# Kernel optimization log

Hardware: AMD Instinct MI355X
Metric: run time of the kernel (lower is better)

The kernel has to match this reference:

```python
import jax, jax.numpy as jnp
import numpy as np

H = 8          # num_heads
EPS = 1e-5     # nn.LayerNorm default eps


def _attn(x, kv, wq, bq, wk, bk, wv, bv, wo, bo):
    # x: [B, Nq, D] queries; kv: [B, Nk, D] keys/values. softmax over keys (dim=-1).
    B, Nq, D = x.shape
    Nk = kv.shape[1]
    d = D // H
    q = (x @ wq + bq).reshape(B, Nq, H, d).transpose(0, 2, 1, 3)   # [B,h,Nq,d]
    k = (kv @ wk + bk).reshape(B, Nk, H, d).transpose(0, 2, 1, 3)  # [B,h,Nk,d]
    v = (kv @ wv + bv).reshape(B, Nk, H, d).transpose(0, 2, 1, 3)  # [B,h,Nk,d]
    scores = jnp.einsum('bhqd,bhkd->bhqk', q, k) * (d ** -0.5)
    a = jax.nn.softmax(scores, axis=-1)                            # softmax_dim='keys'
    ctx = jnp.einsum('bhqk,bhkd->bhqd', a, v)
    ctx = ctx.transpose(0, 2, 1, 3).reshape(B, Nq, D)
    return ctx @ wo + bo


def _ln(x, g, b):
    mu = jnp.mean(x, axis=-1, keepdims=True)
    var = jnp.var(x, axis=-1, keepdims=True)  # biased, matches torch LayerNorm
    return (x - mu) * jax.lax.rsqrt(var + EPS) * g + b


def setup_inputs() -> dict:
    key = jax.random.key(0)
    B, Nq, Nk, D = 2, 2048, 4096, 512
    Hid = 4 * D
    ks = jax.random.split(key, 32)
    s = 0.02
    r = lambda i, shp: jax.random.normal(ks[i], shp, dtype=jnp.float32) * s
    inp = {
        'x': jax.random.normal(ks[0], (B, Nq, D), dtype=jnp.float32),
        'cross': jax.random.normal(ks[1], (B, Nk, D), dtype=jnp.float32),
        # cross-attention projections (stored as [in, out])
        'ca_wq': r(2, (D, D)), 'ca_bq': jnp.zeros((D,), jnp.float32),
        'ca_wk': r(3, (D, D)), 'ca_bk': jnp.zeros((D,), jnp.float32),
        'ca_wv': r(4, (D, D)), 'ca_bv': jnp.zeros((D,), jnp.float32),
        'ca_wo': r(5, (D, D)), 'ca_bo': jnp.zeros((D,), jnp.float32),
        # self-attention projections
        'sa_wq': r(6, (D, D)), 'sa_bq': jnp.zeros((D,), jnp.float32),
        'sa_wk': r(7, (D, D)), 'sa_bk': jnp.zeros((D,), jnp.float32),
        'sa_wv': r(8, (D, D)), 'sa_bv': jnp.zeros((D,), jnp.float32),
        'sa_wo': r(9, (D, D)), 'sa_bo': jnp.zeros((D,), jnp.float32),
        # layer norms
        'ln1_g': jnp.ones((D,), jnp.float32), 'ln1_b': jnp.zeros((D,), jnp.float32),
        'ln2_g': jnp.ones((D,), jnp.float32), 'ln2_b': jnp.zeros((D,), jnp.float32),
        # MLP
        'mlp_w1': r(10, (D, Hid)), 'mlp_b1': jnp.zeros((Hid,), jnp.float32),
        'mlp_w2': r(11, (Hid, D)), 'mlp_b2': jnp.zeros((D,), jnp.float32),
    }
    return inp


def reference(x, cross,
              ca_wq, ca_bq, ca_wk, ca_bk, ca_wv, ca_bv, ca_wo, ca_bo,
              sa_wq, sa_bq, sa_wk, sa_bk, sa_wv, sa_bv, sa_wo, sa_bo,
              ln1_g, ln1_b, ln2_g, ln2_b,
              mlp_w1, mlp_b1, mlp_w2, mlp_b2):
    # a) cross-attention
    xc = _attn(x, cross, ca_wq, ca_bq, ca_wk, ca_bk, ca_wv, ca_bv, ca_wo, ca_bo)
    # b,c) LN then self-attention (Q=K=V=ln1(xc))
    xn = _ln(xc, ln1_g, ln1_b)
    xs = _attn(xn, xn, sa_wq, sa_bq, sa_wk, sa_bk, sa_wv, sa_bv, sa_wo, sa_bo)
    # d) residual
    y = xc + xs
    # e,f) LN + GELU MLP (torch GELU default = exact erf)
    h1 = jax.nn.gelu(_ln(y, ln2_g, ln2_b) @ mlp_w1 + mlp_b1, approximate=False)
    z = h1 @ mlp_w2 + mlp_b2
    # g) residual
    return y + z
```

## Files before the change

kernel.cpp:

```cpp
#include <hip/hip_runtime.h>
#include <math.h>

typedef _Float16 f16;
typedef __attribute__((ext_vector_type(8))) _Float16 f16x8;
typedef __attribute__((ext_vector_type(4))) _Float16 f16x4;
typedef __attribute__((ext_vector_type(4))) float f32x4;
typedef __attribute__((ext_vector_type(2))) __fp16 h16x2;

#define QSCALE 0.1803368801111204f

__device__ __forceinline__ void gl_lds16(const f16* g, f16* l) {
    __builtin_amdgcn_global_load_lds((const __attribute__((address_space(1))) void*)g,
                                     (__attribute__((address_space(3))) void*)l, 16, 0, 0);
}

struct PrepArgs {
    const float* ws[10]; f16* wd[10];
    const float* x; f16* xh;
    const float* cross; f16* ch;
};
__global__ __launch_bounds__(256)
void prep_all(PrepArgs p) {
    __shared__ float t[32][33];
    int bid = blockIdx.x, tid = threadIdx.x;
    if (bid < 4096) {
        const float* W; f16* Wt; int K, N, nx, ky;
        if (bid < 2048) {
            int wi = bid >> 8, tl = bid & 255;
            W = p.ws[wi]; Wt = p.wd[wi]; K = 512; N = 512; nx = tl & 15; ky = tl >> 4;
        } else if (bid < 3072) {
            int tl = bid - 2048;
            W = p.ws[8]; Wt = p.wd[8]; K = 512; N = 2048; nx = tl & 63; ky = tl >> 6;
        } else {
            int tl = bid - 3072;
            W = p.ws[9]; Wt = p.wd[9]; K = 2048; N = 512; nx = tl & 15; ky = tl >> 4;
        }
        int tx = tid & 31, ty = tid >> 5;
        int n0 = nx * 32, k0 = ky * 32;
#pragma unroll
        for (int i = 0; i < 4; i++)
            t[ty + i * 8][tx] = W[(size_t)(k0 + ty + i * 8) * N + n0 + tx];
        __syncthreads();
#pragma unroll
        for (int i = 0; i < 4; i++)
            Wt[(size_t)(n0 + ty + i * 8) * K + k0 + tx] = (f16)t[tx][ty + i * 8];
    } else {
        const float* X; f16* Y; size_t cb;
        if (bid < 6144) { X = p.x; Y = p.xh; cb = bid - 4096; }
        else            { X = p.cross; Y = p.ch; cb = bid - 6144; }
        size_t i = (cb * 256 + tid) * 4;
        f32x4 v = *(const f32x4*)(X + i);
        f16x4 o;
        o[0] = (f16)v[0]; o[1] = (f16)v[1]; o[2] = (f16)v[2]; o[3] = (f16)v[3];
        *(f16x4*)(Y + i) = o;
    }
}

__global__ __launch_bounds__(256)
void transpose_v(const f16* __restrict__ Vh, f16* __restrict__ Vt, int Nk) {
    __shared__ f16 t[64][72];
    int bh = blockIdx.y, k0 = blockIdx.x * 64;
    int tid = threadIdx.x;
    int kr = tid >> 2, dc = (tid & 3) * 16;
    const f16* src = Vh + ((size_t)bh * Nk + k0 + kr) * 64 + dc;
    f16x8 a = *(const f16x8*)src;
    f16x8 b = *(const f16x8*)(src + 8);
    *(f16x8*)&t[kr][dc] = a;
    *(f16x8*)&t[kr][dc + 8] = b;
    __syncthreads();
    int dr = tid >> 2, kc = (tid & 3) * 16;
    f16x8 o0, o1;
#pragma unroll
    for (int j = 0; j < 8; j++) { o0[j] = t[kc + j][dr]; o1[j] = t[kc + 8 + j][dr]; }
    f16* dst = Vt + ((size_t)bh * 64 + dr) * Nk + k0 + kc;
    *(f16x8*)dst = o0;
    *(f16x8*)(dst + 8) = o1;
}

__global__ __launch_bounds__(128)
void layernorm_f16(const float* __restrict__ X, const float* __restrict__ g,
                   const float* __restrict__ bta, f16* __restrict__ Y)
{
    __shared__ float red[4];
    int row = blockIdx.x;
    int tid = threadIdx.x;
    const float* x = X + (size_t)row * 512;
    f32x4 v = *(const f32x4*)(x + tid * 4);
    float s  = v[0] + v[1] + v[2] + v[3];
    float ss = v[0] * v[0] + v[1] * v[1] + v[2] * v[2] + v[3] * v[3];
#pragma unroll
    for (int m = 1; m < 64; m <<= 1) {
        s  += __shfl_xor(s, m, 64);
        ss += __shfl_xor(ss, m, 64);
    }
    int wave = tid >> 6, lane = tid & 63;
    if (lane == 0) { red[wave * 2] = s; red[wave * 2 + 1] = ss; }
    __syncthreads();
    s = red[0] + red[2]; ss = red[1] + red[3];
    float mu  = s * (1.0f / 512);
    float var = ss * (1.0f / 512) - mu * mu;
    float inv = rsqrtf(var + 1e-5f);
    f32x4 gv = *(const f32x4*)(g + tid * 4);
    f32x4 bv = *(const f32x4*)(bta + tid * 4);
    f16x4 o;
#pragma unroll
    for (int i = 0; i < 4; i++) o[i] = (f16)((v[i] - mu) * inv * gv[i] + bv[i]);
    *(f16x4*)(Y + (size_t)row * 512 + tid * 4) = o;
}

__global__ __launch_bounds__(256)
void gemm_f16(const f16* __restrict__ A, const f16* __restrict__ Wt,
              const float* __restrict__ b0, const float* __restrict__ b1,
              const float* __restrict__ b2, const float* __restrict__ res,
              float* __restrict__ Cf32, f16* __restrict__ C16,
              f16* __restrict__ hm0, f16* __restrict__ hm1, f16* __restrict__ hm2,
              int N, int K, int NBshift, int fused, int act, float s0)
{
    __shared__ __align__(16) f16 As[2][128 * 64];
    __shared__ __align__(16) f16 Bs[2][128 * 64];
    int tid = threadIdx.x, lane = tid & 63, wave = tid >> 6;
    int quad = lane >> 4, ln16 = lane & 15;
    int wm = wave >> 1, wn = wave & 1;
    int bm0 = blockIdx.y * 128, bn0 = blockIdx.x * 128;

    f32x4 acc[4][4];
#pragma unroll
    for (int i = 0; i < 4; i++)
#pragma unroll
        for (int j = 0; j < 4; j++) acc[i][j] = (f32x4){0.f, 0.f, 0.f, 0.f};

    const f16* ag[4]; const f16* bg[4]; int Loff[4];
#pragma unroll
    for (int j = 0; j < 4; j++) {
        int L = tid + j * 256;
        int row = L >> 3, cc = (L & 7) ^ (row & 7);
        ag[j] = A  + (size_t)(bm0 + row) * K + cc * 8;
        bg[j] = Wt + (size_t)(bn0 + row) * K + cc * 8;
        Loff[j] = L * 8;
    }
    int sw0 = (quad ^ (ln16 & 7)) * 8, sw1 = ((4 + quad) ^ (ln16 & 7)) * 8;

#pragma unroll
    for (int j = 0; j < 4; j++) { gl_lds16(ag[j], &As[0][Loff[j]]); gl_lds16(bg[j], &Bs[0][Loff[j]]); }
#pragma unroll
    for (int j = 0; j < 4; j++) { ag[j] += 64; bg[j] += 64; }

    int cur = 0;
    for (int kt = 0; kt < K; kt += 64) {
        __syncthreads();
        if (kt + 64 < K) {
            int nxt = cur ^ 1;
#pragma unroll
            for (int j = 0; j < 4; j++) { gl_lds16(ag[j], &As[nxt][Loff[j]]); gl_lds16(bg[j], &Bs[nxt][Loff[j]]); }
#pragma unroll
            for (int j = 0; j < 4; j++) { ag[j] += 64; bg[j] += 64; }
        }
        const f16* Ac = As[cur]; const f16* Bc = Bs[cur];
#pragma unroll
        for (int h = 0; h < 2; h++) {
            int sw = h ? sw1 : sw0;
            f16x8 af[4], bf[4];
#pragma unroll
            for (int mt = 0; mt < 4; mt++)
                af[mt] = *(const f16x8*)&Ac[(wm * 64 + mt * 16 + ln16) * 64 + sw];
#pragma unroll
            for (int nt = 0; nt < 4; nt++)
                bf[nt] = *(const f16x8*)&Bc[(wn * 64 + nt * 16 + ln16) * 64 + sw];
#pragma unroll
            for (int mt = 0; mt < 4; mt++)
#pragma unroll
                for (int nt = 0; nt < 4; nt++)
                    acc[mt][nt] = __builtin_amdgcn_mfma_f32_16x16x32_f16(af[mt], bf[nt], acc[mt][nt], 0, 0, 0);
        }
        cur ^= 1;
    }

    int NB = 1 << NBshift;
#pragma unroll
    for (int mt = 0; mt < 4; mt++) {
#pragma unroll
        for (int nt = 0; nt < 4; nt++) {
            int row = bm0 + wm * 64 + mt * 16 + quad * 4;
            int col = bn0 + wn * 64 + nt * 16 + ln16;
            float bv;
            if (fused) {
                int seg = col >> 9;
                const float* bp = seg == 0 ? b0 : (seg == 1 ? b1 : b2);
                bv = bp[col & 511];
            } else bv = b0[col];
#pragma unroll
            for (int i = 0; i < 4; i++) {
                int r = row + i;
                float v = acc[mt][nt][i] + bv;
                size_t idx = (size_t)r * N + col;
                if (res) v += res[idx];
                if (act) v = 0.5f * v * (1.0f + erff(v * 0.70710678118654752f));
                if (Cf32) Cf32[idx] = v;
                if (C16) C16[idx] = (f16)v;
                if (hm0) {
                    int seg = col >> 9;
                    f16* hp = seg == 0 ? hm0 : (seg == 1 ? hm1 : hm2);
                    float vv = seg == 0 ? v * s0 : v;
                    int hh = (col >> 6) & 7, d = col & 63;
                    int bt = r >> NBshift, rr = r & (NB - 1);
                    hp[(((size_t)bt * 8 + hh) * NB + rr) * 64 + d] = (f16)vv;
                }
            }
        }
    }
}

__global__ __launch_bounds__(256)
void gemm64(const f16* __restrict__ A, const f16* __restrict__ Wt,
            const float* __restrict__ bias, const float* __restrict__ res,
            float* __restrict__ Cf32, f16* __restrict__ hm0,
            int N, int K, int NBshift, float s0)
{
    __shared__ __align__(16) f16 As[2][64 * 64];
    __shared__ __align__(16) f16 Bs[2][64 * 64];
    int tid = threadIdx.x, lane = tid & 63, wave = tid >> 6;
    int quad = lane >> 4, ln16 = lane & 15;
    int wm = wave >> 1, wn = wave & 1;
    int bm0 = blockIdx.y * 64, bn0 = blockIdx.x * 64;

    f32x4 acc[2][2];
#pragma unroll
    for (int i = 0; i < 2; i++)
#pragma unroll
        for (int j = 0; j < 2; j++) acc[i][j] = (f32x4){0.f, 0.f, 0.f, 0.f};

    const f16* ag[2]; const f16* bg[2]; int Loff[2];
#pragma unroll
    for (int j = 0; j < 2; j++) {
        int L = tid + j * 256;
        int row = L >> 3, cc = (L & 7) ^ (row & 7);
        ag[j] = A  + (size_t)(bm0 + row) * K + cc * 8;
        bg[j] = Wt + (size_t)(bn0 + row) * K + cc * 8;
        Loff[j] = L * 8;
    }
    int sw0 = (quad ^ (ln16 & 7)) * 8, sw1 = ((4 + quad) ^ (ln16 & 7)) * 8;

#pragma unroll
    for (int j = 0; j < 2; j++) { gl_lds16(ag[j], &As[0][Loff[j]]); gl_lds16(bg[j], &Bs[0][Loff[j]]); }
#pragma unroll
    for (int j = 0; j < 2; j++) { ag[j] += 64; bg[j] += 64; }

    int cur = 0;
    for (int kt = 0; kt < K; kt += 64) {
        __syncthreads();
        if (kt + 64 < K) {
            int nxt = cur ^ 1;
#pragma unroll
            for (int j = 0; j < 2; j++) { gl_lds16(ag[j], &As[nxt][Loff[j]]); gl_lds16(bg[j], &Bs[nxt][Loff[j]]); }
#pragma unroll
            for (int j = 0; j < 2; j++) { ag[j] += 64; bg[j] += 64; }
        }
        const f16* Ac = As[cur]; const f16* Bc = Bs[cur];
#pragma unroll
        for (int h = 0; h < 2; h++) {
            int sw = h ? sw1 : sw0;
            f16x8 af[2], bf[2];
#pragma unroll
            for (int mt = 0; mt < 2; mt++)
                af[mt] = *(const f16x8*)&Ac[(wm * 32 + mt * 16 + ln16) * 64 + sw];
#pragma unroll
            for (int nt = 0; nt < 2; nt++)
                bf[nt] = *(const f16x8*)&Bc[(wn * 32 + nt * 16 + ln16) * 64 + sw];
#pragma unroll
            for (int mt = 0; mt < 2; mt++)
#pragma unroll
                for (int nt = 0; nt < 2; nt++)
                    acc[mt][nt] = __builtin_amdgcn_mfma_f32_16x16x32_f16(af[mt], bf[nt], acc[mt][nt], 0, 0, 0);
        }
        cur ^= 1;
    }

    int NB = 1 << NBshift;
#pragma unroll
    for (int mt = 0; mt < 2; mt++) {
#pragma unroll
        for (int nt = 0; nt < 2; nt++) {
            int row = bm0 + wm * 32 + mt * 16 + quad * 4;
            int col = bn0 + wn * 32 + nt * 16 + ln16;
            float bv = bias[col];
#pragma unroll
            for (int i = 0; i < 4; i++) {
                int r = row + i;
                float v = acc[mt][nt][i] + bv;
                size_t idx = (size_t)r * N + col;
                if (res) v += res[idx];
                if (Cf32) Cf32[idx] = v;
                if (hm0) {
                    int hh = (col >> 6) & 7, d = col & 63;
                    int bt = r >> NBshift, rr = r & (NB - 1);
                    hm0[(((size_t)bt * 8 + hh) * NB + rr) * 64 + d] = (f16)(v * s0);
                }
            }
        }
    }
}

__global__ __launch_bounds__(512, 4)
void attention_split(const f16* __restrict__ Qh, const f16* __restrict__ Kh,
                     const f16* __restrict__ Vt, f16* __restrict__ Op,
                     float* __restrict__ Lsum, int Nk, int nsp_log)
{
    __shared__ __align__(16) f16 Kt[2][64 * 64];
    __shared__ __align__(16) f16 Vs[2][64 * 64];
    int z = blockIdx.z, b = z >> nsp_log, sp = z & ((1 << nsp_log) - 1);
    int h = blockIdx.y, bh = b * 8 + h;
    int Nkh = Nk >> nsp_log;
    int tid = threadIdx.x, lane = tid & 63, wave = tid >> 6;
    int quad = lane >> 4, ln16 = lane & 15, l7 = ln16 & 7;
    int qrow0 = blockIdx.x * 256 + wave * 32;

    f16x8 qf[2][2];
#pragma unroll
    for (int qh = 0; qh < 2; qh++)
#pragma unroll
        for (int dh = 0; dh < 2; dh++)
            qf[qh][dh] = *(const f16x8*)(Qh + ((size_t)bh * 2048 + qrow0 + qh * 16 + ln16) * 64
                                         + dh * 32 + quad * 8);
    f16x4 ones4;
#pragma unroll
    for (int j = 0; j < 4; j++) ones4[j] = (f16)1.0f;

    f32x4 oacc[2][4], aol[2];
#pragma unroll
    for (int qh = 0; qh < 2; qh++) {
        aol[qh] = (f32x4){0.f, 0.f, 0.f, 0.f};
#pragma unroll
        for (int dt = 0; dt < 4; dt++) oacc[qh][dt] = (f32x4){0.f, 0.f, 0.f, 0.f};
    }

    const f16* kb = Kh + ((size_t)bh * Nk + sp * Nkh) * 64;
    const f16* vb = Vt + (size_t)bh * 64 * Nk + sp * Nkh;

    const f16* kg; const f16* vg; int Lo;
    {
        int L = tid;
        int row = L >> 3, cc = (L & 7) ^ (row & 7);
        kg = kb + (size_t)row * 64 + cc * 8;
        vg = vb + (size_t)row * Nk + cc * 8;
        Lo = L * 8;
    }

    int koff[4][2], voff16[4][4];
#pragma unroll
    for (int nt = 0; nt < 4; nt++)
#pragma unroll
        for (int dh = 0; dh < 2; dh++)
            koff[nt][dh] = (nt * 16 + ln16) * 64 + ((dh * 4 + quad) ^ l7) * 8;
#pragma unroll
    for (int dt = 0; dt < 4; dt++)
#pragma unroll
        for (int nt = 0; nt < 4; nt++)
            voff16[dt][nt] = (dt * 16 + ln16) * 64 + (((nt * 2 + (quad >> 1)) ^ l7) * 8) + (quad & 1) * 4;

    gl_lds16(kg, &Kt[0][Lo]);
    gl_lds16(vg, &Vs[0][Lo]);
    kg += 64 * 64; vg += 64;

    int cur = 0;
    for (int kt = 0; kt < Nkh; kt += 64) {
        __syncthreads();
        if (kt + 64 < Nkh) {
            int nxt = cur ^ 1;
            gl_lds16(kg, &Kt[nxt][Lo]);
            gl_lds16(vg, &Vs[nxt][Lo]);
            kg += 64 * 64; vg += 64;
        }
        const f16* Ktc = Kt[cur]; const f16* Vsc = Vs[cur];

        f16x4 pk[2][4];
        {
            f16x8 kf[4][2];
#pragma unroll
            for (int nt = 0; nt < 4; nt++)
#pragma unroll
                for (int dh = 0; dh < 2; dh++)
                    kf[nt][dh] = *(const f16x8*)&Ktc[koff[nt][dh]];
#pragma unroll
            for (int qh = 0; qh < 2; qh++)
#pragma unroll
                for (int nt = 0; nt < 4; nt++) {
                    f32x4 zz = (f32x4){0.f, 0.f, 0.f, 0.f};
                    zz = __builtin_amdgcn_mfma_f32_16x16x32_f16(kf[nt][0], qf[qh][0], zz, 0, 0, 0);
                    zz = __builtin_amdgcn_mfma_f32_16x16x32_f16(kf[nt][1], qf[qh][1], zz, 0, 0, 0);
                    h16x2 pa = __builtin_amdgcn_cvt_pkrtz(exp2f(zz[0]), exp2f(zz[1]));
                    h16x2 pb = __builtin_amdgcn_cvt_pkrtz(exp2f(zz[2]), exp2f(zz[3]));
                    union { h16x2 h[2]; f16x4 v; } u;
                    u.h[0] = pa; u.h[1] = pb;
                    pk[qh][nt] = u.v;
                }
        }
        {
            f16x4 vf[4][4];
#pragma unroll
            for (int dt = 0; dt < 4; dt++)
#pragma unroll
                for (int nt = 0; nt < 4; nt++)
                    vf[dt][nt] = *(const f16x4*)&Vsc[voff16[dt][nt]];
#pragma unroll
            for (int qh = 0; qh < 2; qh++) {
#pragma unroll
                for (int nt = 0; nt < 4; nt++)
                    aol[qh] = __builtin_amdgcn_mfma_f32_16x16x16f16(ones4, pk[qh][nt], aol[qh], 0, 0, 0);
#pragma unroll
                for (int dt = 0; dt < 4; dt++)
#pragma unroll
                    for (int nt = 0; nt < 4; nt++)
                        oacc[qh][dt] = __builtin_amdgcn_mfma_f32_16x16x16f16(vf[dt][nt], pk[qh][nt], oacc[qh][dt], 0, 0, 0);
            }
        }
        cur ^= 1;
    }

#pragma unroll
    for (int qh = 0; qh < 2; qh++) {
        size_t rowb = ((size_t)(sp * 16 + bh) * 2048 + qrow0 + qh * 16 + ln16) * 64;
#pragma unroll
        for (int dt = 0; dt < 4; dt++) {
            f16x4 o4;
#pragma unroll
            for (int i = 0; i < 4; i++) o4[i] = (f16)oacc[qh][dt][i];
            *(f16x4*)&Op[rowb + dt * 16 + quad * 4] = o4;
        }
        if (quad == 0)
            Lsum[(size_t)(sp * 16 + bh) * 2048 + qrow0 + qh * 16 + ln16] = aol[qh][0];
    }
}

__global__ __launch_bounds__(256)
void attn_combine(const f16* __restrict__ Op, const float* __restrict__ Lsum,
                  f16* __restrict__ O, int nsplit)
{
    int t = blockIdx.x * 256 + threadIdx.x;
    int d = t & 63;
    int q = (t >> 6) & 2047;
    int bh = t >> 17;
    int b = bh >> 3, h = bh & 7;
    float l = 0.f, val = 0.f;
#pragma unroll 4
    for (int s = 0; s < nsplit; s++) {
        l   += Lsum[(size_t)(s * 16 + bh) * 2048 + q];
        val += (float)Op[((size_t)(s * 16 + bh) * 2048 + q) * 64 + d];
    }
    O[((size_t)b * 2048 + q) * 512 + h * 64 + d] = (f16)(val / l);
}

extern "C" void kernel_launch(void* const* d_in, const int* in_sizes, int n_in,
                              void* d_out, int out_size, void* d_ws, size_t ws_size,
                              hipStream_t stream)
{
    (void)in_sizes; (void)n_in; (void)out_size; (void)ws_size;
    const float* x      = (const float*)d_in[0];
    const float* cross  = (const float*)d_in[1];
    const float* ca_wq  = (const float*)d_in[2];
    const float* ca_bq  = (const float*)d_in[3];
    const float* ca_wk  = (const float*)d_in[4];
    const float* ca_bk  = (const float*)d_in[5];
    const float* ca_wv  = (const float*)d_in[6];
    const float* ca_bv  = (const float*)d_in[7];
    const float* ca_wo  = (const float*)d_in[8];
    const float* ca_bo  = (const float*)d_in[9];
    const float* sa_wq  = (const float*)d_in[10];
    const float* sa_bq  = (const float*)d_in[11];
    const float* sa_wk  = (const float*)d_in[12];
    const float* sa_bk  = (const float*)d_in[13];
    const float* sa_wv  = (const float*)d_in[14];
    const float* sa_bv  = (const float*)d_in[15];
    const float* sa_wo  = (const float*)d_in[16];
    const float* sa_bo  = (const float*)d_in[17];
    const float* ln1_g  = (const float*)d_in[18];
    const float* ln1_b  = (const float*)d_in[19];
    const float* ln2_g  = (const float*)d_in[20];
    const float* ln2_b  = (const float*)d_in[21];
    const float* mlp_w1 = (const float*)d_in[22];
    const float* mlp_b1 = (const float*)d_in[23];
    const float* mlp_w2 = (const float*)d_in[24];
    const float* mlp_b2 = (const float*)d_in[25];
    float* out = (float*)d_out;

    float* XC = (float*)d_ws;
    float* Yb = XC + 2097152;
    f16* fb   = (f16*)(Yb + 2097152);
    f16* xh     = fb;
    f16* crossh = xh + 2097152;
    f16* xnh    = crossh + 4194304;
    f16* xn2h   = xnh + 2097152;
    f16* Qh     = xn2h + 2097152;
    f16* Kh     = Qh + 2097152;
    f16* Vh     = Kh + 4194304;
    f16* Vtb    = Vh + 4194304;
    f16* ctxh   = Vtb + 4194304;
    f16* h1h    = ctxh + 2097152;
    f16* t_caq  = h1h + 8388608;
    f16* t_cak  = t_caq + 262144;
    f16* t_cav  = t_cak + 262144;
    f16* t_cao  = t_cav + 262144;
    f16* t_saq  = t_cao + 262144;
    f16* t_sak  = t_saq + 262144;
    f16* t_sav  = t_sak + 262144;
    f16* t_sao  = t_sav + 262144;
    f16* t_w1   = t_sao + 262144;
    f16* t_w2   = t_w1 + 1048576;
    float* Lsum = (float*)(t_w2 + 1048576);

    f16* OpX     = (f16*)d_ws;
    float* LsumX = (float*)xn2h;

    PrepArgs pa;
    pa.ws[0] = ca_wq; pa.wd[0] = t_caq;
    pa.ws[1] = ca_wk; pa.wd[1] = t_cak;
    pa.ws[2] = ca_wv; pa.wd[2] = t_cav;
    pa.ws[3] = ca_wo; pa.wd[3] = t_cao;
    pa.ws[4] = sa_wq; pa.wd[4] = t_saq;
    pa.ws[5] = sa_wk; pa.wd[5] = t_sak;
    pa.ws[6] = sa_wv; pa.wd[6] = t_sav;
    pa.ws[7] = sa_wo; pa.wd[7] = t_sao;
    pa.ws[8] = mlp_w1; pa.wd[8] = t_w1;
    pa.ws[9] = mlp_w2; pa.wd[9] = t_w2;
    pa.x = x; pa.xh = xh; pa.cross = cross; pa.ch = crossh;
    prep_all<<<10240, 256, 0, stream>>>(pa);

    gemm64<<<dim3(8, 64), 256, 0, stream>>>(xh, t_caq, ca_bq, nullptr, nullptr, Qh,
                                            512, 512, 11, QSCALE);
    gemm_f16<<<dim3(8, 64), 256, 0, stream>>>(crossh, t_cak, ca_bk, ca_bv, nullptr, nullptr,
        nullptr, nullptr, Kh, Vh, nullptr, 1024, 512, 12, 1, 0, 1.0f);
    transpose_v<<<dim3(64, 16), 256, 0, stream>>>(Vh, Vtb, 4096);
    attention_split<<<dim3(8, 8, 16), 512, 0, stream>>>(Qh, Kh, Vtb, OpX, LsumX, 4096, 3);
    attn_combine<<<8192, 256, 0, stream>>>(OpX, LsumX, ctxh, 8);
    gemm64<<<dim3(8, 64), 256, 0, stream>>>(ctxh, t_cao, ca_bo, nullptr, XC, nullptr,
                                            512, 512, 11, 1.0f);
    layernorm_f16<<<4096, 128, 0, stream>>>(XC, ln1_g, ln1_b, xnh);
    gemm_f16<<<dim3(12, 32), 256, 0, stream>>>(xnh, t_saq, sa_bq, sa_bk, sa_bv, nullptr,
        nullptr, nullptr, Qh, Kh, Vh, 1536, 512, 11, 1, 0, QSCALE);
    transpose_v<<<dim3(32, 16), 256, 0, stream>>>(Vh, Vtb, 2048);
    attention_split<<<dim3(8, 8, 8), 512, 0, stream>>>(Qh, Kh, Vtb, h1h, Lsum, 2048, 2);
    attn_combine<<<8192, 256, 0, stream>>>(h1h, Lsum, ctxh, 4);
    gemm64<<<dim3(8, 64), 256, 0, stream>>>(ctxh, t_sao, sa_bo, XC, Yb, nullptr,
                                            512, 512, 11, 1.0f);
    layernorm_f16<<<4096, 128, 0, stream>>>(Yb, ln2_g, ln2_b, xn2h);
    gemm_f16<<<dim3(16, 32), 256, 0, stream>>>(xn2h, t_w1, mlp_b1, nullptr, nullptr, nullptr,
        nullptr, h1h, nullptr, nullptr, nullptr, 2048, 512, 11, 0, 1, 1.0f);
    gemm64<<<dim3(8, 64), 256, 0, stream>>>(h1h, t_w2, mlp_b2, Yb, out, nullptr,
                                            512, 2048, 11, 1.0f);
}
```

Before: 368.0 us.

## Fuse V transpose into projection GEMM and switch attention to 32x32 MFMA

The K/V and QKV projection GEMMs now write V directly in transposed head-major layout, which removes both transpose_v launches and their extra global round trip. The attention kernel is rebuilt around 32x32x16 MFMA tiles. P is passed between the QK and PV products through lane shuffles, and the row sum is taken in scalar registers instead of through a ones-vector MFMA. The cross-attention split factor drops from 8 to 4, which lowers the combine work but leaves fewer blocks. The transposed-V epilogue stores strided 4-element vectors, which may coalesce less well.

```diff
diff --git a/kernel.cpp b/kernel.cpp
--- a/kernel.cpp
+++ b/kernel.cpp
@@ -5,6 +5,7 @@
 typedef __attribute__((ext_vector_type(8))) _Float16 f16x8;
 typedef __attribute__((ext_vector_type(4))) _Float16 f16x4;
 typedef __attribute__((ext_vector_type(4))) float f32x4;
+typedef __attribute__((ext_vector_type(16))) float f32x16;
 typedef __attribute__((ext_vector_type(2))) __fp16 h16x2;
 
 #define QSCALE 0.1803368801111204f
@@ -56,27 +57,6 @@
     }
 }
 
-__global__ __launch_bounds__(256)
-void transpose_v(const f16* __restrict__ Vh, f16* __restrict__ Vt, int Nk) {
-    __shared__ f16 t[64][72];
-    int bh = blockIdx.y, k0 = blockIdx.x * 64;
-    int tid = threadIdx.x;
-    int kr = tid >> 2, dc = (tid & 3) * 16;
-    const f16* src = Vh + ((size_t)bh * Nk + k0 + kr) * 64 + dc;
-    f16x8 a = *(const f16x8*)src;
-    f16x8 b = *(const f16x8*)(src + 8);
-    *(f16x8*)&t[kr][dc] = a;
-    *(f16x8*)&t[kr][dc + 8] = b;
-    __syncthreads();
-    int dr = tid >> 2, kc = (tid & 3) * 16;
-    f16x8 o0, o1;
-#pragma unroll
-    for (int j = 0; j < 8; j++) { o0[j] = t[kc + j][dr]; o1[j] = t[kc + 8 + j][dr]; }
-    f16* dst = Vt + ((size_t)bh * 64 + dr) * Nk + k0 + kc;
-    *(f16x8*)dst = o0;
-    *(f16x8*)(dst + 8) = o1;
-}
-
 __global__ __launch_bounds__(128)
 void layernorm_f16(const float* __restrict__ X, const float* __restrict__ g,
                    const float* __restrict__ bta, f16* __restrict__ Y)
@@ -114,6 +94,7 @@
               const float* __restrict__ b2, const float* __restrict__ res,
               float* __restrict__ Cf32, f16* __restrict__ C16,
               f16* __restrict__ hm0, f16* __restrict__ hm1, f16* __restrict__ hm2,
+              f16* __restrict__ vtp, int vseg,
               int N, int K, int NBshift, int fused, int act, float s0)
 {
     __shared__ __align__(16) f16 As[2][128 * 64];
@@ -188,22 +169,31 @@
                 const float* bp = seg == 0 ? b0 : (seg == 1 ? b1 : b2);
                 bv = bp[col & 511];
             } else bv = b0[col];
-#pragma unroll
-            for (int i = 0; i < 4; i++) {
-                int r = row + i;
-                float v = acc[mt][nt][i] + bv;
-                size_t idx = (size_t)r * N + col;
-                if (res) v += res[idx];
-                if (act) v = 0.5f * v * (1.0f + erff(v * 0.70710678118654752f));
-                if (Cf32) Cf32[idx] = v;
-                if (C16) C16[idx] = (f16)v;
-                if (hm0) {
-                    int seg = col >> 9;
-                    f16* hp = seg == 0 ? hm0 : (seg == 1 ? hm1 : hm2);
-                    float vv = seg == 0 ? v * s0 : v;
-                    int hh = (col >> 6) & 7, d = col & 63;
-                    int bt = r >> NBshift, rr = r & (NB - 1);
-                    hp[(((size_t)bt * 8 + hh) * NB + rr) * 64 + d] = (f16)vv;
+            int seg = col >> 9;
+            if (vtp && seg == vseg) {
+                int hh = (col >> 6) & 7, d = col & 63;
+                int bt = row >> NBshift, rr = row & (NB - 1);
+                f16x4 o4;
+#pragma unroll
+                for (int i = 0; i < 4; i++) o4[i] = (f16)(acc[mt][nt][i] + bv);
+                *(f16x4*)&vtp[(((size_t)bt * 8 + hh) * 64 + d) * NB + rr] = o4;
+            } else {
+#pragma unroll
+                for (int i = 0; i < 4; i++) {
+                    int r = row + i;
+                    float v = acc[mt][nt][i] + bv;
+                    size_t idx = (size_t)r * N + col;
+                    if (res) v += res[idx];
+                    if (act) v = 0.5f * v * (1.0f + erff(v * 0.70710678118654752f));
+                    if (Cf32) Cf32[idx] = v;
+                    if (C16) C16[idx] = (f16)v;
+                    if (hm0) {
+                        f16* hp = seg == 0 ? hm0 : (seg == 1 ? hm1 : hm2);
+                        float vv = seg == 0 ? v * s0 : v;
+                        int hh = (col >> 6) & 7, d = col & 63;
+                        int bt = r >> NBshift, rr = r & (NB - 1);
+                        hp[(((size_t)bt * 8 + hh) * NB + rr) * 64 + d] = (f16)vv;
+                    }
                 }
             }
         }
@@ -308,30 +298,23 @@
     __shared__ __align__(16) f16 Kt[2][64 * 64];
     __shared__ __align__(16) f16 Vs[2][64 * 64];
     int z = blockIdx.z, b = z >> nsp_log, sp = z & ((1 << nsp_log) - 1);
-    int h = blockIdx.y, bh = b * 8 + h;
+    int h8 = blockIdx.y, bh = b * 8 + h8;
     int Nkh = Nk >> nsp_log;
     int tid = threadIdx.x, lane = tid & 63, wave = tid >> 6;
-    int quad = lane >> 4, ln16 = lane & 15, l7 = ln16 & 7;
+    int lq = lane & 31, hh = lane >> 5, l7 = lane & 7;
     int qrow0 = blockIdx.x * 256 + wave * 32;
 
-    f16x8 qf[2][2];
-#pragma unroll
-    for (int qh = 0; qh < 2; qh++)
-#pragma unroll
-        for (int dh = 0; dh < 2; dh++)
-            qf[qh][dh] = *(const f16x8*)(Qh + ((size_t)bh * 2048 + qrow0 + qh * 16 + ln16) * 64
-                                         + dh * 32 + quad * 8);
-    f16x4 ones4;
-#pragma unroll
-    for (int j = 0; j < 4; j++) ones4[j] = (f16)1.0f;
-
-    f32x4 oacc[2][4], aol[2];
-#pragma unroll
-    for (int qh = 0; qh < 2; qh++) {
-        aol[qh] = (f32x4){0.f, 0.f, 0.f, 0.f};
-#pragma unroll
-        for (int dt = 0; dt < 4; dt++) oacc[qh][dt] = (f32x4){0.f, 0.f, 0.f, 0.f};
-    }
+    f16x8 qf[4];
+#pragma unroll
+    for (int s = 0; s < 4; s++)
+        qf[s] = *(const f16x8*)(Qh + ((size_t)bh * 2048 + qrow0 + lq) * 64 + s * 16 + hh * 8);
+
+    f32x16 oacc[2];
+#pragma unroll
+    for (int db = 0; db < 2; db++)
+#pragma unroll
+        for (int r = 0; r < 16; r++) oacc[db][r] = 0.f;
+    float lacc = 0.f;
 
     const f16* kb = Kh + ((size_t)bh * Nk + sp * Nkh) * 64;
     const f16* vb = Vt + (size_t)bh * 64 * Nk + sp * Nkh;
@@ -345,17 +328,12 @@
         Lo = L * 8;
     }
 
-    int koff[4][2], voff16[4][4];
-#pragma unroll
-    for (int nt = 0; nt < 4; nt++)
-#pragma unroll
-        for (int dh = 0; dh < 2; dh++)
-            koff[nt][dh] = (nt * 16 + ln16) * 64 + ((dh * 4 + quad) ^ l7) * 8;
-#pragma unroll
-    for (int dt = 0; dt < 4; dt++)
-#pragma unroll
-        for (int nt = 0; nt < 4; nt++)
-            voff16[dt][nt] = (dt * 16 + ln16) * 64 + (((nt * 2 + (quad >> 1)) ^ l7) * 8) + (quad & 1) * 4;
+    int off[2][4];
+#pragma unroll
+    for (int g = 0; g < 2; g++)
+#pragma unroll
+        for (int s = 0; s < 4; s++)
+            off[g][s] = (g * 32 + lq) * 64 + (((2 * s + hh) ^ l7) * 8);
 
     gl_lds16(kg, &Kt[0][Lo]);
     gl_lds16(vg, &Vs[0][Lo]);
@@ -372,63 +350,62 @@
         }
         const f16* Ktc = Kt[cur]; const f16* Vsc = Vs[cur];
 
-        f16x4 pk[2][4];
-        {
-            f16x8 kf[4][2];
-#pragma unroll
-            for (int nt = 0; nt < 4; nt++)
-#pragma unroll
-                for (int dh = 0; dh < 2; dh++)
-                    kf[nt][dh] = *(const f16x8*)&Ktc[koff[nt][dh]];
-#pragma unroll
-            for (int qh = 0; qh < 2; qh++)
-#pragma unroll
-                for (int nt = 0; nt < 4; nt++) {
-                    f32x4 zz = (f32x4){0.f, 0.f, 0.f, 0.f};
-                    zz = __builtin_amdgcn_mfma_f32_16x16x32_f16(kf[nt][0], qf[qh][0], zz, 0, 0, 0);
-                    zz = __builtin_amdgcn_mfma_f32_16x16x32_f16(kf[nt][1], qf[qh][1], zz, 0, 0, 0);
-                    h16x2 pa = __builtin_amdgcn_cvt_pkrtz(exp2f(zz[0]), exp2f(zz[1]));
-                    h16x2 pb = __builtin_amdgcn_cvt_pkrtz(exp2f(zz[2]), exp2f(zz[3]));
-                    union { h16x2 h[2]; f16x4 v; } u;
-                    u.h[0] = pa; u.h[1] = pb;
-                    pk[qh][nt] = u.v;
+#pragma unroll
+        for (int kbk = 0; kbk < 2; kbk++) {
+            f32x16 c;
+#pragma unroll
+            for (int r = 0; r < 16; r++) c[r] = 0.f;
+#pragma unroll
+            for (int s = 0; s < 4; s++) {
+                f16x8 kf = *(const f16x8*)&Ktc[off[kbk][s]];
+                c = __builtin_amdgcn_mfma_f32_32x32x16_f16(kf, qf[s], c, 0, 0, 0);
+            }
+            int pr[8];
+#pragma unroll
+            for (int m = 0; m < 8; m++) {
+                float e0 = exp2f(c[2 * m]), e1 = exp2f(c[2 * m + 1]);
+                lacc += e0 + e1;
+                union { h16x2 h; int i; } u;
+                u.h = __builtin_amdgcn_cvt_pkrtz(e0, e1);
+                pr[m] = u.i;
+            }
+#pragma unroll
+            for (int t = 0; t < 2; t++) {
+                int p0 = pr[4 * t + 0], p1 = pr[4 * t + 1];
+                int p2 = pr[4 * t + 2], p3 = pr[4 * t + 3];
+                int s0 = __shfl_xor(p0, 32, 64);
+                int s1 = __shfl_xor(p1, 32, 64);
+                int s2 = __shfl_xor(p2, 32, 64);
+                int s3 = __shfl_xor(p3, 32, 64);
+                union { int i[4]; f16x8 v; } bu;
+                bu.i[0] = hh ? s2 : p0;
+                bu.i[1] = hh ? s3 : p1;
+                bu.i[2] = hh ? p2 : s0;
+                bu.i[3] = hh ? p3 : s1;
+                int ks = kbk * 2 + t;
+#pragma unroll
+                for (int db = 0; db < 2; db++) {
+                    f16x8 vf = *(const f16x8*)&Vsc[off[db][ks]];
+                    oacc[db] = __builtin_amdgcn_mfma_f32_32x32x16_f16(vf, bu.v, oacc[db], 0, 0, 0);
                 }
-        }
-        {
-            f16x4 vf[4][4];
-#pragma unroll
-            for (int dt = 0; dt < 4; dt++)
-#pragma unroll
-                for (int nt = 0; nt < 4; nt++)
-                    vf[dt][nt] = *(const f16x4*)&Vsc[voff16[dt][nt]];
-#pragma unroll
-            for (int qh = 0; qh < 2; qh++) {
-#pragma unroll
-                for (int nt = 0; nt < 4; nt++)
-                    aol[qh] = __builtin_amdgcn_mfma_f32_16x16x16f16(ones4, pk[qh][nt], aol[qh], 0, 0, 0);
-#pragma unroll
-                for (int dt = 0; dt < 4; dt++)
-#pragma unroll
-                    for (int nt = 0; nt < 4; nt++)
-                        oacc[qh][dt] = __builtin_amdgcn_mfma_f32_16x16x16f16(vf[dt][nt], pk[qh][nt], oacc[qh][dt], 0, 0, 0);
             }
         }
         cur ^= 1;
     }
 
-#pragma unroll
-    for (int qh = 0; qh < 2; qh++) {
-        size_t rowb = ((size_t)(sp * 16 + bh) * 2048 + qrow0 + qh * 16 + ln16) * 64;
-#pragma unroll
-        for (int dt = 0; dt < 4; dt++) {
+    float ltot = lacc + __shfl_xor(lacc, 32, 64);
+    size_t rowb = ((size_t)(sp * 16 + bh) * 2048 + qrow0 + lq) * 64;
+#pragma unroll
+    for (int db = 0; db < 2; db++)
+#pragma unroll
+        for (int rq = 0; rq < 4; rq++) {
             f16x4 o4;
 #pragma unroll
-            for (int i = 0; i < 4; i++) o4[i] = (f16)oacc[qh][dt][i];
-            *(f16x4*)&Op[rowb + dt * 16 + quad * 4] = o4;
-        }
-        if (quad == 0)
-            Lsum[(size_t)(sp * 16 + bh) * 2048 + qrow0 + qh * 16 + ln16] = aol[qh][0];
-    }
+            for (int i = 0; i < 4; i++) o4[i] = (f16)oacc[db][rq * 4 + i];
+            *(f16x4*)&Op[rowb + db * 32 + rq * 8 + hh * 4] = o4;
+        }
+    if (hh == 0)
+        Lsum[(size_t)(sp * 16 + bh) * 2048 + qrow0 + lq] = ltot;
 }
 
 __global__ __launch_bounds__(256)
@@ -507,9 +484,6 @@
     f16* t_w2   = t_w1 + 1048576;
     float* Lsum = (float*)(t_w2 + 1048576);
 
-    f16* OpX     = (f16*)d_ws;
-    float* LsumX = (float*)xn2h;
-
     PrepArgs pa;
     pa.ws[0] = ca_wq; pa.wd[0] = t_caq;
     pa.ws[1] = ca_wk; pa.wd[1] = t_cak;
@@ -527,23 +501,21 @@
     gemm64<<<dim3(8, 64), 256, 0, stream>>>(xh, t_caq, ca_bq, nullptr, nullptr, Qh,
                                             512, 512, 11, QSCALE);
     gemm_f16<<<dim3(8, 64), 256, 0, stream>>>(crossh, t_cak, ca_bk, ca_bv, nullptr, nullptr,
-        nullptr, nullptr, Kh, Vh, nullptr, 1024, 512, 12, 1, 0, 1.0f);
-    transpose_v<<<dim3(64, 16), 256, 0, stream>>>(Vh, Vtb, 4096);
-    attention_split<<<dim3(8, 8, 16), 512, 0, stream>>>(Qh, Kh, Vtb, OpX, LsumX, 4096, 3);
-    attn_combine<<<8192, 256, 0, stream>>>(OpX, LsumX, ctxh, 8);
+        nullptr, nullptr, Kh, nullptr, nullptr, Vtb, 1, 1024, 512, 12, 1, 0, 1.0f);
+    attention_split<<<dim3(8, 8, 8), 512, 0, stream>>>(Qh, Kh, Vtb, h1h, Lsum, 4096, 2);
+    attn_combine<<<8192, 256, 0, stream>>>(h1h, Lsum, ctxh, 4);
     gemm64<<<dim3(8, 64), 256, 0, stream>>>(ctxh, t_cao, ca_bo, nullptr, XC, nullptr,
                                             512, 512, 11, 1.0f);
     layernorm_f16<<<4096, 128, 0, stream>>>(XC, ln1_g, ln1_b, xnh);
     gemm_f16<<<dim3(12, 32), 256, 0, stream>>>(xnh, t_saq, sa_bq, sa_bk, sa_bv, nullptr,
-        nullptr, nullptr, Qh, Kh, Vh, 1536, 512, 11, 1, 0, QSCALE);
-    transpose_v<<<dim3(32, 16), 256, 0, stream>>>(Vh, Vtb, 2048);
+        nullptr, nullptr, Qh, Kh, nullptr, Vtb, 2, 1536, 512, 11, 1, 0, QSCALE);
     attention_split<<<dim3(8, 8, 8), 512, 0, stream>>>(Qh, Kh, Vtb, h1h, Lsum, 2048, 2);
     attn_combine<<<8192, 256, 0, stream>>>(h1h, Lsum, ctxh, 4);
     gemm64<<<dim3(8, 64), 256, 0, stream>>>(ctxh, t_sao, sa_bo, XC, Yb, nullptr,
                                             512, 512, 11, 1.0f);
     layernorm_f16<<<4096, 128, 0, stream>>>(Yb, ln2_g, ln2_b, xn2h);
     gemm_f16<<<dim3(16, 32), 256, 0, stream>>>(xn2h, t_w1, mlp_b1, nullptr, nullptr, nullptr,
-        nullptr, h1h, nullptr, nullptr, nullptr, 2048, 512, 11, 0, 1, 1.0f);
+        nullptr, h1h, nullptr, nullptr, nullptr, nullptr, 0, 2048, 512, 11, 0, 1, 1.0f);
     gemm64<<<dim3(8, 64), 256, 0, stream>>>(h1h, t_w2, mlp_b2, Yb, out, nullptr,
                                             512, 2048, 11, 1.0f);
 }
```

Result: no change. 364.5 us (-1.0%).
